# Optimization experiments

Measured on AMD Instinct MI355X. Metric: run time of the kernel, lower is better.

The kernel has to match this reference:

```python
import jax, jax.numpy as jnp
import numpy as np

B, H, W, DIM, HEADS = 4, 32, 32, 768, 12
HD = DIM // HEADS


def setup_inputs() -> dict:
    key = jax.random.key(0)
    ks = jax.random.split(key, 5)
    return {
        "x": jax.random.normal(ks[0], (B, H, W, DIM), jnp.float32),
        "qkv_w": jax.random.normal(ks[1], (3 * DIM, DIM), jnp.float32) * 0.02,
        "qkv_b": jnp.zeros((3 * DIM,), jnp.float32),
        "proj_w": jax.random.normal(ks[2], (DIM, DIM), jnp.float32) * 0.02,
        "proj_b": jnp.zeros((DIM,), jnp.float32),
        "rel_pos_h": jax.random.normal(ks[3], (2 * H - 1, HD), jnp.float32) * 0.02,
        "rel_pos_w": jax.random.normal(ks[4], (2 * W - 1, HD), jnp.float32) * 0.02,
    }


def reference(x, qkv_w, qkv_b, proj_w, proj_b, rel_pos_h, rel_pos_w):
    b, h, w, dim = x.shape
    heads = HEADS
    hd = dim // heads
    n = h * w
    scale = hd ** -0.5

    xf = x.reshape(b, n, dim)
    qkv = xf @ qkv_w.T + qkv_b                          # [b, n, 3*dim]
    qkv = qkv.reshape(b, n, 3, heads, hd)
    qkv = jnp.transpose(qkv, (2, 0, 3, 1, 4)).reshape(3, b * heads, n, hd)
    q, k, v = qkv[0], qkv[1], qkv[2]                    # [b*heads, n, hd]

    # decomposed relative position bias (q_size == k_size, no interpolation)
    idx_h = jnp.arange(h)[:, None] - jnp.arange(h)[None, :] + (h - 1)
    idx_w = jnp.arange(w)[:, None] - jnp.arange(w)[None, :] + (w - 1)
    Rh = rel_pos_h[idx_h]                               # [h, h, hd]
    Rw = rel_pos_w[idx_w]                               # [w, w, hd]
    r_q = q.reshape(b * heads, h, w, hd)
    rel_h = jnp.einsum('bhwc,hkc->bhwk', r_q, Rh)       # [bH, h, w, h]
    rel_w = jnp.einsum('bhwc,wkc->bhwk', r_q, Rw)       # [bH, h, w, w]
    bias = (rel_h[:, :, :, :, None] + rel_w[:, :, :, None, :]).reshape(b * heads, n, n)

    attn = jax.nn.softmax(jnp.einsum('bnd,bmd->bnm', q * scale, k) + bias, axis=-1)
    out = jnp.einsum('bnm,bmd->bnd', attn, v)           # [b*heads, n, hd]
    out = out.reshape(b, heads, n, hd).transpose(0, 2, 1, 3).reshape(b, n, dim)
    out = out @ proj_w.T + proj_b
    return out.reshape(b, h, w, dim)
```

## Files before the change

kernel.cpp:

```cpp
#include <hip/hip_runtime.h>

#define DEV_INLINE static __device__ __forceinline__

typedef __attribute__((ext_vector_type(8))) short bf16x8;
typedef __attribute__((ext_vector_type(4))) float f32x4;
typedef __attribute__((ext_vector_type(16))) float f32x16;

DEV_INLINE unsigned short f2bf(float f) {
  union { float f; unsigned int u; } v; v.f = f;
  unsigned int u = v.u;
  u += 0x7FFFu + ((u >> 16) & 1u);
  return (unsigned short)(u >> 16);
}
DEV_INLINE float bf2f(unsigned short h) {
  union { unsigned int u; float f; } v; v.u = ((unsigned int)h) << 16; return v.f;
}

__global__ __launch_bounds__(256) void cvt_f32_bf16(const float* __restrict__ in,
                                                    unsigned short* __restrict__ out, int n4) {
  int i = blockIdx.x * 256 + threadIdx.x;
  if (i >= n4) return;
  float4 v = reinterpret_cast<const float4*>(in)[i];
  ushort4 o;
  o.x = f2bf(v.x); o.y = f2bf(v.y); o.z = f2bf(v.z); o.w = f2bf(v.w);
  reinterpret_cast<ushort4*>(out)[i] = o;
}

template <int MODE>
__global__ __launch_bounds__(256) void gemm_bf16(const unsigned short* __restrict__ A,
                                                 const unsigned short* __restrict__ Bw,
                                                 const float* __restrict__ bias,
                                                 float* __restrict__ outF,
                                                 unsigned short* __restrict__ qo,
                                                 unsigned short* __restrict__ ko,
                                                 unsigned short* __restrict__ vo) {
  __shared__ unsigned short As[3][128 * 32];
  __shared__ unsigned short Bs[3][128 * 32];

  const int tid = threadIdx.x;
  const int lane = tid & 63;
  const int wv = tid >> 6;
  const int wrow = (wv >> 1) * 64;
  const int wcol = (wv & 1) * 64;
  const int m0 = blockIdx.y * 128;
  const int n0 = blockIdx.x * 128;
  const int l15 = lane & 15;
  const int lg = lane >> 4;

  const int srow = lane >> 2;
  const int seg  = (lane & 3) ^ (srow & 3);

  f32x4 acc[4][4];
#pragma unroll
  for (int i = 0; i < 4; ++i)
#pragma unroll
    for (int j = 0; j < 4; ++j) acc[i][j] = (f32x4){0.f, 0.f, 0.f, 0.f};

#define GSTAGE(KT, B)                                                                        \
  do {                                                                                       \
    _Pragma("unroll") for (int pp = 0; pp < 2; ++pp) {                                       \
      int p = wv * 2 + pp;                                   \
      int row = p * 16 + srow;                                                               \
      const unsigned short* ga = &A[(m0 + row) * 768 + (KT) * 32 + seg * 8];                 \
      __builtin_amdgcn_global_load_lds(                                                      \
          (const __attribute__((address_space(1))) unsigned int*)ga,                         \
          (__attribute__((address_space(3))) unsigned int*)&As[B][p * 512], 16, 0, 0);       \
      const unsigned short* gb = &Bw[(n0 + row) * 768 + (KT) * 32 + seg * 8];                \
      __builtin_amdgcn_global_load_lds(                                                      \
          (const __attribute__((address_space(1))) unsigned int*)gb,                         \
          (__attribute__((address_space(3))) unsigned int*)&Bs[B][p * 512], 16, 0, 0);       \
    }                                                                                        \
  } while (0)

  GSTAGE(0, 0);
  GSTAGE(1, 1);

  const int soff = (lg ^ (l15 & 3)) * 8;

#pragma unroll
  for (int kt = 0; kt < 24; ++kt) {
    const int b = kt % 3;
    if (kt < 23) asm volatile("s_waitcnt vmcnt(4)" ::: "memory");
    else         asm volatile("s_waitcnt vmcnt(0)" ::: "memory");
    __builtin_amdgcn_s_barrier();
    asm volatile("" ::: "memory");
    if (kt < 22) GSTAGE(kt + 2, (kt + 2) % 3);

    bf16x8 aF[4], bF[4];
#pragma unroll
    for (int i = 0; i < 4; ++i)
      aF[i] = *reinterpret_cast<const bf16x8*>(&As[b][(wrow + i * 16 + l15) * 32 + soff]);
#pragma unroll
    for (int j = 0; j < 4; ++j)
      bF[j] = *reinterpret_cast<const bf16x8*>(&Bs[b][(wcol + j * 16 + l15) * 32 + soff]);
#pragma unroll
    for (int i = 0; i < 4; ++i)
#pragma unroll
      for (int j = 0; j < 4; ++j)
        acc[i][j] = __builtin_amdgcn_mfma_f32_16x16x32_bf16(aF[i], bF[j], acc[i][j], 0, 0, 0);
  }
#undef GSTAGE

#pragma unroll
  for (int i = 0; i < 4; ++i) {
#pragma unroll
    for (int j = 0; j < 4; ++j) {
#pragma unroll
      for (int r = 0; r < 4; ++r) {
        int row = m0 + wrow + i * 16 + (lane >> 4) * 4 + r;
        int col = n0 + wcol + j * 16 + l15;
        float val = acc[i][j][r] + bias[col];
        if (MODE == 0) {
          int t = col / 768;
          int rem = col - t * 768;
          int head = rem >> 6;
          int c = rem & 63;
          int bb = row >> 10;
          int n = row & 1023;
          if (t == 0) val *= 1.44269504f;
          if (t == 1) val *= 0.125f;
          unsigned short* dst = (t == 0) ? qo : (t == 1) ? ko : vo;
          dst[((bb * 12 + head) * 1024 + n) * 64 + c] = f2bf(val);
        } else {
          outF[row * 768 + col] = val;
        }
      }
    }
  }
}

__global__ __launch_bounds__(256) void vtrans(const unsigned short* __restrict__ vb,
                                              unsigned short* __restrict__ vt) {
  __shared__ unsigned short t[64][72];
  const int n0 = blockIdx.x * 64;
  const int bh = blockIdx.y;
  const int tid = threadIdx.x;
#pragma unroll
  for (int i = 0; i < 4; ++i) {
    int s = tid + i * 256;
    int row = s >> 4, c4 = (s & 15) * 4;
    *reinterpret_cast<ushort4*>(&t[row][c4]) =
        *reinterpret_cast<const ushort4*>(&vb[(bh * 1024 + n0 + row) * 64 + c4]);
  }
  __syncthreads();
#pragma unroll
  for (int i = 0; i < 4; ++i) {
    int s = tid + i * 256;
    int d = s >> 4, n4 = (s & 15) * 4;
    ushort4 o;
    o.x = t[n4 + 0][d]; o.y = t[n4 + 1][d]; o.z = t[n4 + 2][d]; o.w = t[n4 + 3][d];
    *reinterpret_cast<ushort4*>(&vt[(bh * 64 + d) * 1024 + n0 + n4]) = o;
  }
}

DEV_INLINE f32x4 mfma16(bf16x8 a, bf16x8 b, f32x4 c) {
  return __builtin_amdgcn_mfma_f32_16x16x32_bf16(a, b, c, 0, 0, 0);
}

__global__ __launch_bounds__(64) void rel_mfma16(const unsigned short* __restrict__ q,
                                                 const float* __restrict__ rph,
                                                 const float* __restrict__ rpw,
                                                 unsigned short* __restrict__ relwb,
                                                 float* __restrict__ relh) {
  __shared__ unsigned short qs[32 * 72];
  __shared__ unsigned short rhh[32 * 72], rhl[32 * 72];
  __shared__ unsigned short rwh[64 * 72], rwl[64 * 72];
  __shared__ float relh_s[32 * 36];
  __shared__ unsigned short relw_s[32 * 40];

  const int lane = threadIdx.x;
  const int l15 = lane & 15;
  const int lg = lane >> 4;
  const int qh = blockIdx.x;
  const int bh = blockIdx.y;

#pragma unroll
  for (int it = 0; it < 4; ++it) {
    int s = lane + it * 64;
    int row = s >> 3, ch = s & 7;
    *reinterpret_cast<int4*>(&qs[row * 72 + ch * 8]) =
        *reinterpret_cast<const int4*>(&q[(bh * 1024 + qh * 32 + row) * 64 + ch * 8]);
  }
#pragma unroll
  for (int it = 0; it < 8; ++it) {
    int s = lane + it * 64;
    int row = s >> 4, c4 = (s & 15) * 4;
    float4 v = *reinterpret_cast<const float4*>(&rph[(qh + row) * 64 + c4]);
    ushort4 h, l;
    h.x = f2bf(v.x); l.x = f2bf(v.x - bf2f(h.x));
    h.y = f2bf(v.y); l.y = f2bf(v.y - bf2f(h.y));
    h.z = f2bf(v.z); l.z = f2bf(v.z - bf2f(h.z));
    h.w = f2bf(v.w); l.w = f2bf(v.w - bf2f(h.w));
    *reinterpret_cast<ushort4*>(&rhh[row * 72 + c4]) = h;
    *reinterpret_cast<ushort4*>(&rhl[row * 72 + c4]) = l;
  }
#pragma unroll
  for (int it = 0; it < 16; ++it) {
    int s = lane + it * 64;
    int row = s >> 4, c4 = (s & 15) * 4;
    float4 v = (float4){0.f, 0.f, 0.f, 0.f};
    if (row < 63) v = *reinterpret_cast<const float4*>(&rpw[row * 64 + c4]);
    ushort4 h, l;
    h.x = f2bf(v.x); l.x = f2bf(v.x - bf2f(h.x));
    h.y = f2bf(v.y); l.y = f2bf(v.y - bf2f(h.y));
    h.z = f2bf(v.z); l.z = f2bf(v.z - bf2f(h.z));
    h.w = f2bf(v.w); l.w = f2bf(v.w - bf2f(h.w));
    *reinterpret_cast<ushort4*>(&rwh[row * 72 + c4]) = h;
    *reinterpret_cast<ushort4*>(&rwl[row * 72 + c4]) = l;
  }
  __syncthreads();

  const int k0 = lg * 8, k1 = 32 + lg * 8;
  bf16x8 fq[2][2], fhh[2][2], fhl[2][2], fwh[4][2], fwl[4][2];
#pragma unroll
  for (int t = 0; t < 2; ++t) {
    fq[t][0]  = *reinterpret_cast<const bf16x8*>(&qs[(t * 16 + l15) * 72 + k0]);
    fq[t][1]  = *reinterpret_cast<const bf16x8*>(&qs[(t * 16 + l15) * 72 + k1]);
    fhh[t][0] = *reinterpret_cast<const bf16x8*>(&rhh[(t * 16 + l15) * 72 + k0]);
    fhh[t][1] = *reinterpret_cast<const bf16x8*>(&rhh[(t * 16 + l15) * 72 + k1]);
    fhl[t][0] = *reinterpret_cast<const bf16x8*>(&rhl[(t * 16 + l15) * 72 + k0]);
    fhl[t][1] = *reinterpret_cast<const bf16x8*>(&rhl[(t * 16 + l15) * 72 + k1]);
  }
#pragma unroll
  for (int t = 0; t < 4; ++t) {
    fwh[t][0] = *reinterpret_cast<const bf16x8*>(&rwh[(t * 16 + l15) * 72 + k0]);
    fwh[t][1] = *reinterpret_cast<const bf16x8*>(&rwh[(t * 16 + l15) * 72 + k1]);
    fwl[t][0] = *reinterpret_cast<const bf16x8*>(&rwl[(t * 16 + l15) * 72 + k0]);
    fwl[t][1] = *reinterpret_cast<const bf16x8*>(&rwl[(t * 16 + l15) * 72 + k1]);
  }

  f32x4 ah[2][2];
#pragma unroll
  for (int i = 0; i < 2; ++i)
#pragma unroll
    for (int jj = 0; jj < 2; ++jj) {
      f32x4 a = (f32x4){0.f, 0.f, 0.f, 0.f};
      a = mfma16(fhh[i][0], fq[jj][0], a);
      a = mfma16(fhh[i][1], fq[jj][1], a);
      a = mfma16(fhl[i][0], fq[jj][0], a);
      a = mfma16(fhl[i][1], fq[jj][1], a);
      ah[i][jj] = a;
    }
  f32x4 aw[2][4];
#pragma unroll
  for (int i = 0; i < 2; ++i)
#pragma unroll
    for (int jj = 0; jj < 4; ++jj) {
      f32x4 a = (f32x4){0.f, 0.f, 0.f, 0.f};
      a = mfma16(fq[i][0], fwh[jj][0], a);
      a = mfma16(fq[i][1], fwh[jj][1], a);
      a = mfma16(fq[i][0], fwl[jj][0], a);
      a = mfma16(fq[i][1], fwl[jj][1], a);
      aw[i][jj] = a;
    }

#pragma unroll
  for (int i = 0; i < 2; ++i)
#pragma unroll
    for (int jj = 0; jj < 2; ++jj)
#pragma unroll
      for (int r = 0; r < 4; ++r) {
        int t = i * 16 + lg * 4 + r;
        int qw = jj * 16 + l15;
        relh_s[qw * 36 + 31 - t] = ah[i][jj][r];
      }
#pragma unroll
  for (int i = 0; i < 2; ++i)
#pragma unroll
    for (int jj = 0; jj < 4; ++jj)
#pragma unroll
      for (int r = 0; r < 4; ++r) {
        int qw = i * 16 + lg * 4 + r;
        int d = jj * 16 + l15;
        int kw = qw + 31 - d;
        if (kw >= 0 && kw < 32) relw_s[qw * 40 + kw] = f2bf(aw[i][jj][r]);
      }
  __syncthreads();

#pragma unroll
  for (int it = 0; it < 4; ++it) {
    int s = lane + it * 64;
    int row = s >> 3, c4 = (s & 7) * 4;
    *reinterpret_cast<float4*>(&relh[(bh * 1024 + qh * 32 + row) * 32 + c4]) =
        *reinterpret_cast<const float4*>(&relh_s[row * 36 + c4]);
  }
#pragma unroll
  for (int it = 0; it < 2; ++it) {
    int s = lane + it * 64;
    int row = s >> 2, ch = s & 3;
    *reinterpret_cast<int4*>(&relwb[(bh * 1024 + qh * 32 + row) * 32 + ch * 8]) =
        *reinterpret_cast<const int4*>(&relw_s[row * 40 + ch * 8]);
  }
}

DEV_INLINE f32x16 mfma32(bf16x8 a, bf16x8 b, f32x16 c) {
  return __builtin_amdgcn_mfma_f32_32x32x16_bf16(a, b, c, 0, 0, 0);
}

DEV_INLINE bf16x8 make_pa(const float* p) {
  unsigned int W0, W1, W2, W3;
  asm("v_cvt_pk_bf16_f32 %0, %1, %2" : "=v"(W0) : "v"(p[0]), "v"(p[1]));
  asm("v_cvt_pk_bf16_f32 %0, %1, %2" : "=v"(W1) : "v"(p[2]), "v"(p[3]));
  asm("v_cvt_pk_bf16_f32 %0, %1, %2" : "=v"(W2) : "v"(p[4]), "v"(p[5]));
  asm("v_cvt_pk_bf16_f32 %0, %1, %2" : "=v"(W3) : "v"(p[6]), "v"(p[7]));
  asm("v_permlane32_swap_b32 %0, %1" : "+v"(W0), "+v"(W2));
  asm("v_permlane32_swap_b32 %0, %1" : "+v"(W1), "+v"(W3));
  union { unsigned int w[4]; bf16x8 v; } u;
  u.w[0] = W0; u.w[1] = W1; u.w[2] = W2; u.w[3] = W3;
  return u.v;
}

__global__ __launch_bounds__(128) void attn2(const unsigned short* __restrict__ kg,
                                             const unsigned short* __restrict__ vtg,
                                             const unsigned short* __restrict__ qg,
                                             const unsigned short* __restrict__ relwb,
                                             const float* __restrict__ relh,
                                             unsigned short* __restrict__ ao) {
  __shared__ unsigned short k_lin[3][64 * 64];
  __shared__ unsigned short v_lin[3][64 * 64];

  const int tid = threadIdx.x;
  const int lane = tid & 63;
  const int wv = tid >> 6;
  const int l31 = lane & 31;
  const int hi = lane >> 5;

  const int bid = blockIdx.x;
  const int swz = (bid & 7) * 96 + (bid >> 3);
  const int bh = swz >> 4;
  const int qt = swz & 15;
  const int q0 = qt * 64 + wv * 32;

  bf16x8 qf[6];
  {
    const unsigned short* qrow = &qg[(bh * 1024 + q0 + l31) * 64 + hi * 8];
#pragma unroll
    for (int c = 0; c < 4; ++c)
      qf[c] = *reinterpret_cast<const bf16x8*>(&qrow[c * 16]);
    const unsigned short* wrow = &relwb[(bh * 1024 + q0 + l31) * 32 + hi * 8];
    qf[4] = *reinterpret_cast<const bf16x8*>(&wrow[0]);
    qf[5] = *reinterpret_cast<const bf16x8*>(&wrow[16]);
  }

  bf16x8 ohf0, ohf1;
  {
    int t0 = l31 - 8 * hi;
    int t1 = l31 - 16 - 8 * hi;
    union { unsigned int w[4]; bf16x8 v; } u0, u1;
#pragma unroll
    for (int w = 0; w < 4; ++w) {
      u0.w[w] = (t0 >= 0 && (t0 >> 1) == w) ? ((t0 & 1) ? 0x3F800000u : 0x3F80u) : 0u;
      u1.w[w] = (t1 >= 0 && (t1 >> 1) == w) ? ((t1 & 1) ? 0x3F800000u : 0x3F80u) : 0u;
    }
    ohf0 = u0.v; ohf1 = u1.v;
  }

  float bhr[32];
  {
    const float* rhrow = &relh[(bh * 1024 + q0 + l31) * 32];
#pragma unroll
    for (int i = 0; i < 8; ++i) {
      float4 t4 = *reinterpret_cast<const float4*>(&rhrow[i * 4]);
      bhr[i * 4 + 0] = t4.x; bhr[i * 4 + 1] = t4.y;
      bhr[i * 4 + 2] = t4.z; bhr[i * 4 + 3] = t4.w;
    }
  }

  f32x16 O0, O1;
#pragma unroll
  for (int r = 0; r < 16; ++r) { O0[r] = 0.f; O1[r] = 0.f; }
  float m_r = -3.0e38f, l_r = 0.f;

  const int srow = lane >> 3;
  const int scb = (lane & 7) ^ srow;
  const int rsw = l31 & 7;

#define STAGE(KT, B)                                                                       \
  do {                                                                                     \
    _Pragma("unroll") for (int pp = 0; pp < 4; ++pp) {                                     \
      int p = wv * 4 + pp;                                                                 \
      int row = p * 8 + srow;                                                              \
      const unsigned short* gk = &kg[(bh * 1024 + (KT) * 64 + row) * 64 + scb * 8];        \
      __builtin_amdgcn_global_load_lds(                                                    \
          (const __attribute__((address_space(1))) unsigned int*)gk,                       \
          (__attribute__((address_space(3))) unsigned int*)&k_lin[B][p * 512], 16, 0, 0);  \
      const unsigned short* gv = &vtg[(bh * 64 + row) * 1024 + (KT) * 64 + scb * 8];       \
      __builtin_amdgcn_global_load_lds(                                                    \
          (const __attribute__((address_space(1))) unsigned int*)gv,                       \
          (__attribute__((address_space(3))) unsigned int*)&v_lin[B][p * 512], 16, 0, 0);  \
    }                                                                                      \
  } while (0)

  STAGE(0, 0);
  STAGE(1, 1);

#pragma unroll
  for (int kt = 0; kt < 16; ++kt) {
    const int b = kt % 3;
    if (kt < 15) asm volatile("s_waitcnt vmcnt(8)" ::: "memory");
    else         asm volatile("s_waitcnt vmcnt(0)" ::: "memory");
    __builtin_amdgcn_s_barrier();
    asm volatile("" ::: "memory");
    if (kt < 14) STAGE(kt + 2, (kt + 2) % 3);

    float bh0 = bhr[2 * kt], bh1 = bhr[2 * kt + 1];

    f32x16 s0, s1;
#pragma unroll
    for (int r = 0; r < 16; ++r) { s0[r] = 0.f; s1[r] = 0.f; }
    {
      const unsigned short* kb0 = &k_lin[b][l31 * 64];
      const unsigned short* kb1 = &k_lin[b][(32 + l31) * 64];
      __builtin_amdgcn_s_setprio(1);
#pragma unroll
      for (int c = 0; c < 4; ++c) {
        int cb = ((2 * c + hi) ^ rsw) * 8;
        s0 = mfma32(*reinterpret_cast<const bf16x8*>(&kb0[cb]), qf[c], s0);
        s1 = mfma32(*reinterpret_cast<const bf16x8*>(&kb1[cb]), qf[c], s1);
      }
      s0 = mfma32(ohf0, qf[4], s0);
      s0 = mfma32(ohf1, qf[5], s0);
      s1 = mfma32(ohf0, qf[4], s1);
      s1 = mfma32(ohf1, qf[5], s1);
      __builtin_amdgcn_s_setprio(0);
    }

    float pm0 = s0[0], pm1 = s1[0];
#pragma unroll
    for (int r = 1; r < 16; ++r) { pm0 = fmaxf(pm0, s0[r]); pm1 = fmaxf(pm1, s1[r]); }
    float pmax = fmaxf(pm0 + bh0, pm1 + bh1);
    pmax = fmaxf(pmax, __shfl_xor(pmax, 32));

    if (!__all(pmax <= m_r + 11.5f)) {
      float mnew = fmaxf(m_r, pmax);
      float corr = __builtin_amdgcn_exp2f(m_r - mnew);
      m_r = mnew;
      l_r *= corr;
#pragma unroll
      for (int r = 0; r < 16; ++r) {
        int cr = ((r & 3) + 8 * (r >> 2) + 4 * hi) << 2;
        float c2 = __int_as_float(__builtin_amdgcn_ds_bpermute(cr, __float_as_int(corr)));
        O0[r] *= c2;
        O1[r] *= c2;
      }
    }

    float mb0 = m_r - bh0, mb1 = m_r - bh1;
    float p0[16], p1[16];
    float ps = 0.f;
#pragma unroll
    for (int r = 0; r < 16; ++r) { p0[r] = __builtin_amdgcn_exp2f(s0[r] - mb0); ps += p0[r]; }
#pragma unroll
    for (int r = 0; r < 16; ++r) { p1[r] = __builtin_amdgcn_exp2f(s1[r] - mb1); ps += p1[r]; }
    ps += __shfl_xor(ps, 32);
    l_r += ps;

    bf16x8 pa0 = make_pa(p0 + 0);
    bf16x8 pa1 = make_pa(p0 + 8);
    bf16x8 pa2 = make_pa(p1 + 0);
    bf16x8 pa3 = make_pa(p1 + 8);

    const unsigned short* vb0 = &v_lin[b][l31 * 64];
    const unsigned short* vb1 = &v_lin[b][(32 + l31) * 64];
    __builtin_amdgcn_s_setprio(1);
#pragma unroll
    for (int c = 0; c < 4; ++c) {
      bf16x8 pac = (c == 0) ? pa0 : (c == 1) ? pa1 : (c == 2) ? pa2 : pa3;
      int cb = ((2 * c + hi) ^ rsw) * 8;
      O0 = mfma32(pac, *reinterpret_cast<const bf16x8*>(&vb0[cb]), O0);
      O1 = mfma32(pac, *reinterpret_cast<const bf16x8*>(&vb1[cb]), O1);
    }
    __builtin_amdgcn_s_setprio(0);
  }
#undef STAGE

  float invl = 1.f / l_r;
  const int bb = bh / 12, head = bh % 12;
#pragma unroll
  for (int r = 0; r < 16; ++r) {
    int crow = (r & 3) + 8 * (r >> 2) + 4 * hi;
    float il = __int_as_float(__builtin_amdgcn_ds_bpermute(crow << 2, __float_as_int(invl)));
    int n = q0 + crow;
    unsigned short* dst = &ao[(bb * 1024 + n) * 768 + head * 64];
    dst[l31] = f2bf(O0[r] * il);
    dst[32 + l31] = f2bf(O1[r] * il);
  }
}

extern "C" void kernel_launch(void* const* d_in, const int* in_sizes, int n_in,
                              void* d_out, int out_size, void* d_ws, size_t ws_size,
                              hipStream_t stream) {
  const float* x      = (const float*)d_in[0];
  const float* qkv_w  = (const float*)d_in[1];
  const float* qkv_b  = (const float*)d_in[2];
  const float* proj_w = (const float*)d_in[3];
  const float* proj_b = (const float*)d_in[4];
  const float* rph    = (const float*)d_in[5];
  const float* rpw    = (const float*)d_in[6];
  float* out = (float*)d_out;

  char* ws = (char*)d_ws;
  unsigned short* xb    = (unsigned short*)(ws);
  float*          relh  = (float*)(ws);
  unsigned short* wqkv  = (unsigned short*)(ws + 6291456);
  unsigned short* wproj = (unsigned short*)(ws + 9830400);
  unsigned short* qb    = (unsigned short*)(ws + 11010048);
  unsigned short* kb    = (unsigned short*)(ws + 17301504);
  unsigned short* vb    = (unsigned short*)(ws + 23592960);
  unsigned short* ao    = (unsigned short*)(ws + 23592960);
  unsigned short* vt    = (unsigned short*)(ws + 29884416);
  unsigned short* relwb = (unsigned short*)(ws + 36175872);

  cvt_f32_bf16<<<3072, 256, 0, stream>>>(x, xb, 786432);
  cvt_f32_bf16<<<1728, 256, 0, stream>>>(qkv_w, wqkv, 442368);
  cvt_f32_bf16<<<576, 256, 0, stream>>>(proj_w, wproj, 147456);

  gemm_bf16<0><<<dim3(18, 32), 256, 0, stream>>>(xb, wqkv, qkv_b, nullptr, qb, kb, vb);
  vtrans<<<dim3(16, 48), 256, 0, stream>>>(vb, vt);
  rel_mfma16<<<dim3(32, 48), 64, 0, stream>>>(qb, rph, rpw, relwb, relh);
  attn2<<<768, 128, 0, stream>>>(kb, vt, qb, relwb, relh, ao);
  gemm_bf16<1><<<dim3(6, 32), 256, 0, stream>>>(ao, wproj, proj_b, out, nullptr, nullptr, nullptr);
}
```

Measured before the change: 128.8 us.

## Load K/V fragments directly from global into registers, one wave per block

The attention kernel drops the LDS triple-buffered global_load_lds staging and barriers. Each 64-thread block now handles 32 query rows and reads K and V^T fragments straight from global memory into registers, prefetching the next K tile and the next relative-height bias pair during compute. The grid doubles to 1536 single-wave blocks, which removes the cross-wave sync. The cost is that K/V data is no longer shared between two waves through LDS, so global and L2 traffic doubles, and the V loads are issued in the same iteration they are used, which may expose latency.

```diff
diff --git a/kernel.cpp b/kernel.cpp
--- a/kernel.cpp
+++ b/kernel.cpp
@@ -310,26 +310,21 @@
   return u.v;
 }
 
-__global__ __launch_bounds__(128) void attn2(const unsigned short* __restrict__ kg,
-                                             const unsigned short* __restrict__ vtg,
-                                             const unsigned short* __restrict__ qg,
-                                             const unsigned short* __restrict__ relwb,
-                                             const float* __restrict__ relh,
-                                             unsigned short* __restrict__ ao) {
-  __shared__ unsigned short k_lin[3][64 * 64];
-  __shared__ unsigned short v_lin[3][64 * 64];
-
-  const int tid = threadIdx.x;
-  const int lane = tid & 63;
-  const int wv = tid >> 6;
+__global__ __launch_bounds__(64) void attn2(const unsigned short* __restrict__ kg,
+                                            const unsigned short* __restrict__ vtg,
+                                            const unsigned short* __restrict__ qg,
+                                            const unsigned short* __restrict__ relwb,
+                                            const float* __restrict__ relh,
+                                            unsigned short* __restrict__ ao) {
+  const int lane = threadIdx.x;
   const int l31 = lane & 31;
   const int hi = lane >> 5;
 
   const int bid = blockIdx.x;
-  const int swz = (bid & 7) * 96 + (bid >> 3);
-  const int bh = swz >> 4;
-  const int qt = swz & 15;
-  const int q0 = qt * 64 + wv * 32;
+  const int swz = (bid & 7) * 192 + (bid >> 3);
+  const int bh = swz >> 5;
+  const int qt = swz & 31;
+  const int q0 = qt * 32;
 
   bf16x8 qf[6];
   {
@@ -355,74 +350,64 @@
     ohf0 = u0.v; ohf1 = u1.v;
   }
 
-  float bhr[32];
-  {
-    const float* rhrow = &relh[(bh * 1024 + q0 + l31) * 32];
-#pragma unroll
-    for (int i = 0; i < 8; ++i) {
-      float4 t4 = *reinterpret_cast<const float4*>(&rhrow[i * 4]);
-      bhr[i * 4 + 0] = t4.x; bhr[i * 4 + 1] = t4.y;
-      bhr[i * 4 + 2] = t4.z; bhr[i * 4 + 3] = t4.w;
-    }
-  }
-
   f32x16 O0, O1;
 #pragma unroll
   for (int r = 0; r < 16; ++r) { O0[r] = 0.f; O1[r] = 0.f; }
   float m_r = -3.0e38f, l_r = 0.f;
 
-  const int srow = lane >> 3;
-  const int scb = (lane & 7) ^ srow;
-  const int rsw = l31 & 7;
-
-#define STAGE(KT, B)                                                                       \
-  do {                                                                                     \
-    _Pragma("unroll") for (int pp = 0; pp < 4; ++pp) {                                     \
-      int p = wv * 4 + pp;                                                                 \
-      int row = p * 8 + srow;                                                              \
-      const unsigned short* gk = &kg[(bh * 1024 + (KT) * 64 + row) * 64 + scb * 8];        \
-      __builtin_amdgcn_global_load_lds(                                                    \
-          (const __attribute__((address_space(1))) unsigned int*)gk,                       \
-          (__attribute__((address_space(3))) unsigned int*)&k_lin[B][p * 512], 16, 0, 0);  \
-      const unsigned short* gv = &vtg[(bh * 64 + row) * 1024 + (KT) * 64 + scb * 8];       \
-      __builtin_amdgcn_global_load_lds(                                                    \
-          (const __attribute__((address_space(1))) unsigned int*)gv,                       \
-          (__attribute__((address_space(3))) unsigned int*)&v_lin[B][p * 512], 16, 0, 0);  \
-    }                                                                                      \
-  } while (0)
-
-  STAGE(0, 0);
-  STAGE(1, 1);
-
-#pragma unroll
+  const unsigned short* kbase = kg + (size_t)bh * 1024 * 64;
+  const unsigned short* vbase = vtg + (size_t)bh * 64 * 1024;
+  const int koffA = l31 * 64 + hi * 8;
+  const int koffB = (32 + l31) * 64 + hi * 8;
+  const int voffA = l31 * 1024 + hi * 8;
+  const int voffB = (32 + l31) * 1024 + hi * 8;
+
+  bf16x8 kf[4][2];
+#pragma unroll
+  for (int c = 0; c < 4; ++c) {
+    kf[c][0] = *reinterpret_cast<const bf16x8*>(&kbase[koffA + c * 16]);
+    kf[c][1] = *reinterpret_cast<const bf16x8*>(&kbase[koffB + c * 16]);
+  }
+
+  const float* rhrow = &relh[(bh * 1024 + q0 + l31) * 32];
+  float2 bhv = *reinterpret_cast<const float2*>(&rhrow[0]);
+
   for (int kt = 0; kt < 16; ++kt) {
-    const int b = kt % 3;
-    if (kt < 15) asm volatile("s_waitcnt vmcnt(8)" ::: "memory");
-    else         asm volatile("s_waitcnt vmcnt(0)" ::: "memory");
-    __builtin_amdgcn_s_barrier();
-    asm volatile("" ::: "memory");
-    if (kt < 14) STAGE(kt + 2, (kt + 2) % 3);
-
-    float bh0 = bhr[2 * kt], bh1 = bhr[2 * kt + 1];
+    const unsigned short* vb = vbase + kt * 64;
+    bf16x8 vf[4][2];
+#pragma unroll
+    for (int c = 0; c < 4; ++c) {
+      vf[c][0] = *reinterpret_cast<const bf16x8*>(&vb[voffA + c * 16]);
+      vf[c][1] = *reinterpret_cast<const bf16x8*>(&vb[voffB + c * 16]);
+    }
+
+    float2 bhv_next = bhv;
+    if (kt < 15) bhv_next = *reinterpret_cast<const float2*>(&rhrow[2 * (kt + 1)]);
+    float bh0 = bhv.x, bh1 = bhv.y;
 
     f32x16 s0, s1;
 #pragma unroll
     for (int r = 0; r < 16; ++r) { s0[r] = 0.f; s1[r] = 0.f; }
+    __builtin_amdgcn_s_setprio(1);
+#pragma unroll
+    for (int c = 0; c < 4; ++c) {
+      s0 = mfma32(kf[c][0], qf[c], s0);
+      s1 = mfma32(kf[c][1], qf[c], s1);
+    }
+    s0 = mfma32(ohf0, qf[4], s0);
+    s0 = mfma32(ohf1, qf[5], s0);
+    s1 = mfma32(ohf0, qf[4], s1);
+    s1 = mfma32(ohf1, qf[5], s1);
+    __builtin_amdgcn_s_setprio(0);
+
     {
-      const unsigned short* kb0 = &k_lin[b][l31 * 64];
-      const unsigned short* kb1 = &k_lin[b][(32 + l31) * 64];
-      __builtin_amdgcn_s_setprio(1);
+      int ktn = (kt < 15) ? kt + 1 : 15;
+      const unsigned short* kb = kbase + ktn * 64 * 64;
 #pragma unroll
       for (int c = 0; c < 4; ++c) {
-        int cb = ((2 * c + hi) ^ rsw) * 8;
-        s0 = mfma32(*reinterpret_cast<const bf16x8*>(&kb0[cb]), qf[c], s0);
-        s1 = mfma32(*reinterpret_cast<const bf16x8*>(&kb1[cb]), qf[c], s1);
+        kf[c][0] = *reinterpret_cast<const bf16x8*>(&kb[koffA + c * 16]);
+        kf[c][1] = *reinterpret_cast<const bf16x8*>(&kb[koffB + c * 16]);
       }
-      s0 = mfma32(ohf0, qf[4], s0);
-      s0 = mfma32(ohf1, qf[5], s0);
-      s1 = mfma32(ohf0, qf[4], s1);
-      s1 = mfma32(ohf1, qf[5], s1);
-      __builtin_amdgcn_s_setprio(0);
     }
 
     float pm0 = s0[0], pm1 = s1[0];
@@ -460,19 +445,17 @@
     bf16x8 pa2 = make_pa(p1 + 0);
     bf16x8 pa3 = make_pa(p1 + 8);
 
-    const unsigned short* vb0 = &v_lin[b][l31 * 64];
-    const unsigned short* vb1 = &v_lin[b][(32 + l31) * 64];
     __builtin_amdgcn_s_setprio(1);
 #pragma unroll
     for (int c = 0; c < 4; ++c) {
       bf16x8 pac = (c == 0) ? pa0 : (c == 1) ? pa1 : (c == 2) ? pa2 : pa3;
-      int cb = ((2 * c + hi) ^ rsw) * 8;
-      O0 = mfma32(pac, *reinterpret_cast<const bf16x8*>(&vb0[cb]), O0);
-      O1 = mfma32(pac, *reinterpret_cast<const bf16x8*>(&vb1[cb]), O1);
+      O0 = mfma32(pac, vf[c][0], O0);
+      O1 = mfma32(pac, vf[c][1], O1);
     }
     __builtin_amdgcn_s_setprio(0);
-  }
-#undef STAGE
+
+    bhv = bhv_next;
+  }
 
   float invl = 1.f / l_r;
   const int bb = bh / 12, head = bh % 12;
@@ -518,6 +501,6 @@
   gemm_bf16<0><<<dim3(18, 32), 256, 0, stream>>>(xb, wqkv, qkv_b, nullptr, qb, kb, vb);
   vtrans<<<dim3(16, 48), 256, 0, stream>>>(vb, vt);
   rel_mfma16<<<dim3(32, 48), 64, 0, stream>>>(qb, rph, rpw, relwb, relh);
-  attn2<<<768, 128, 0, stream>>>(kb, vt, qb, relwb, relh, ao);
+  attn2<<<1536, 64, 0, stream>>>(kb, vt, qb, relwb, relh, ao);
   gemm_bf16<1><<<dim3(6, 32), 256, 0, stream>>>(ao, wproj, proj_b, out, nullptr, nullptr, nullptr);
 }
```

Measured after the change: 131.7 us. 2.3% more time.
